# Performance work log

Hardware: AMD Instinct MI355X
Metric: run time of the kernel (lower is better)

Reference implementation:

```python
import jax, jax.numpy as jnp
import numpy as np

N, E, IN, H, OUT, G = 50000, 800000, 128, 256, 10, 512


def setup_inputs() -> dict:
    key = jax.random.key(0)
    ks = jax.random.split(key, 12)
    def lin(k, fan_in, fan_out):
        s = 1.0 / np.sqrt(fan_in)
        kw, kb = jax.random.split(k)
        W = jax.random.uniform(kw, (fan_in, fan_out), jnp.float32, -s, s)
        b = jax.random.uniform(kb, (fan_out,), jnp.float32, -s, s)
        return W, b
    x = jax.random.normal(ks[0], (N, IN), jnp.float32)
    edge_index = jax.random.randint(ks[1], (2, E), 0, N)
    batch = jnp.sort(jax.random.randint(ks[2], (N,), 0, G))
    W1a, b1a = lin(ks[3], IN, H)
    W1b, b1b = lin(ks[4], H, H)
    W2a, b2a = lin(ks[5], H, H)
    W2b, b2b = lin(ks[6], H, H)
    Wlin, blin = lin(ks[7], H, OUT)
    eps1 = jnp.zeros((), jnp.float32)
    eps2 = jnp.zeros((), jnp.float32)
    return dict(x=x, edge_index=edge_index, batch=batch,
                eps1=eps1, W1a=W1a, b1a=b1a, W1b=W1b, b1b=b1b,
                eps2=eps2, W2a=W2a, b2a=b2a, W2b=W2b, b2b=b2b,
                Wlin=Wlin, blin=blin)


def reference(x, edge_index, batch, eps1, W1a, b1a, W1b, b1b,
              eps2, W2a, b2a, W2b, b2b, Wlin, blin):
    src, dst = edge_index[0], edge_index[1]
    # GINConv 1: h = MLP((1+eps)*x + sum_{j in N(i)} x_j)
    agg = jax.ops.segment_sum(x[src], dst, num_segments=N)  # [N, IN]
    h = (1.0 + eps1) * x + agg
    h = jax.nn.relu(h @ W1a + b1a) @ W1b + b1b              # [N, H]
    h = jax.nn.relu(h)  # (dropout p=0.3 is identity in eval mode)
    # GINConv 2
    agg2 = jax.ops.segment_sum(h[src], dst, num_segments=N)  # [N, H]
    h2 = (1.0 + eps2) * h + agg2
    h2 = jax.nn.relu(h2 @ W2a + b2a) @ W2b + b2b             # [N, H]
    # global mean pool per graph
    psum = jax.ops.segment_sum(h2, batch, num_segments=G)    # [G, H]
    cnt = jax.ops.segment_sum(jnp.ones((N, 1), h2.dtype), batch, num_segments=G)
    pooled = psum / jnp.maximum(cnt, 1.0)
    out = pooled @ Wlin + blin                               # [G, OUT]
    return jax.nn.log_softmax(out, axis=-1)
```

## Files before the change

### kernel.cpp

```cpp
#include <hip/hip_runtime.h>
#include <math.h>
#include <stdint.h>

constexpr int N   = 50000;
constexpr int E   = 800000;
constexpr int IN  = 128;
constexpr int H   = 256;
constexpr int OUT = 10;
constexpr int G   = 512;
constexpr int BSTR = 64;

constexpr int NPART  = 391;
constexpr int SEGCAP = 48;
constexpr int EPB    = 4096;
constexpr int AB     = (E + EPB - 1) / EPB;

typedef __bf16 bf16x8 __attribute__((ext_vector_type(8)));
typedef float  f32x4  __attribute__((ext_vector_type(4)));
typedef float  f32x2  __attribute__((ext_vector_type(2)));

__device__ __forceinline__ float blo(unsigned v) { return __uint_as_float(v << 16); }
__device__ __forceinline__ float bhi(unsigned v) { return __uint_as_float(v & 0xffff0000u); }
__device__ __forceinline__ unsigned short f2b(float f) {
  unsigned u = __float_as_uint(f);
  u += 0x7fffu + ((u >> 16) & 1u);
  return (unsigned short)(u >> 16);
}
__device__ __forceinline__ unsigned packb(float lo, float hi) {
  return (unsigned)f2b(lo) | ((unsigned)f2b(hi) << 16);
}
__device__ __forceinline__ unsigned pk_fp8x4(float a, float b, float c, float d) {
  int r = 0;
  r = __builtin_amdgcn_cvt_pk_fp8_f32(a, b, r, false);
  r = __builtin_amdgcn_cvt_pk_fp8_f32(c, d, r, true);
  return (unsigned)r;
}
__device__ __forceinline__ unsigned char fp8_1(float v) {
  return (unsigned char)(__builtin_amdgcn_cvt_pk_fp8_f32(v, v, 0, false) & 0xff);
}
__device__ __forceinline__ f32x2 upk_fp8(unsigned short s) {
  return __builtin_amdgcn_cvt_pk_f32_fp8((int)s, false);
}


constexpr int XQ_BLOCKS  = (N * IN / 4) / 256;
constexpr int W1A_BLOCKS = (256 * IN) / 256;
constexpr int WH_BLOCKS  = (256 * H) / 256;

__global__ __launch_bounds__(256) void prep_kernel(
    const int* __restrict__ srcp, const int* __restrict__ dstp,
    unsigned* __restrict__ pbuf, int* __restrict__ pcnt,
    const float* __restrict__ x, unsigned* __restrict__ xq,
    const float* __restrict__ W1a, unsigned short* __restrict__ Wt1a,
    const float* __restrict__ W1b, unsigned short* __restrict__ Wt1b,
    const float* __restrict__ W2a, unsigned short* __restrict__ Wt2a,
    const float* __restrict__ W2b, unsigned short* __restrict__ Wt2b) {
  __shared__ int lcur[NPART];
  int b = blockIdx.x;
  int t = threadIdx.x;
  if (b < AB) {
    for (int j = t; j < NPART; j += 256) lcur[j] = 0;
    __syncthreads();
    const int e0 = b * EPB;
#pragma unroll
    for (int r = 0; r < EPB / 1024; ++r) {
      int base = e0 + (r * 256 + t) * 4;
      if (base < E) {
        int4 d4 = *(const int4*)(dstp + base);
        int4 s4 = *(const int4*)(srcp + base);
        int dd[4] = {d4.x, d4.y, d4.z, d4.w};
        int ss[4] = {s4.x, s4.y, s4.z, s4.w};
#pragma unroll
        for (int u = 0; u < 4; ++u) {
          int part = dd[u] >> 7, dl = dd[u] & 127;
          int pos = atomicAdd(&lcur[part], 1);
          if (pos < SEGCAP)
            pbuf[((size_t)part * AB + b) * SEGCAP + pos] =
                ((unsigned)dl << 16) | (unsigned)ss[u];
        }
      }
    }
    __syncthreads();
    for (int j = t; j < NPART; j += 256) pcnt[b * NPART + j] = min(lcur[j], SEGCAP);
    return;
  }
  b -= AB;
  if (b < XQ_BLOCKS) {
    int id = b * 256 + t;
    float4 v = ((const float4*)x)[id];
    xq[id] = pk_fp8x4(v.x, v.y, v.z, v.w);
    return;
  }
  b -= XQ_BLOCKS;
  if (b < W1A_BLOCKS) {
    int id = b * 256 + t;
    int n = id >> 7, k = id & 127;
    Wt1a[id] = f2b(W1a[k * 256 + n]);
    return;
  }
  b -= W1A_BLOCKS;
  const float* Ws;
  unsigned short* Wd;
  if (b < WH_BLOCKS)            { Ws = W1b; Wd = Wt1b; }
  else if (b < 2 * WH_BLOCKS)   { Ws = W2a; Wd = Wt2a; b -= WH_BLOCKS; }
  else                          { Ws = W2b; Wd = Wt2b; b -= 2 * WH_BLOCKS; }
  int id = b * 256 + t;
  int n = id >> 8, k = id & 255;
  Wd[id] = f2b(Ws[k * 256 + n]);
}


__global__ __launch_bounds__(256) void csr_kernel(const unsigned* __restrict__ pbuf,
                                                  const int* __restrict__ pcnt,
                                                  int* __restrict__ deg, int* __restrict__ csre) {
  __shared__ int sa[256], sb[256];
  __shared__ int ldeg[128];
  int p = blockIdx.x;
  int t = threadIdx.x;
  if (t < 128) ldeg[t] = 0;
  sa[t] = (t < AB) ? pcnt[t * NPART + p] : 0;
  __syncthreads();
  int* cur = sa; int* nxt = sb;
#pragma unroll
  for (int off = 1; off < 256; off <<= 1) {
    nxt[t] = cur[t] + ((t >= off) ? cur[t - off] : 0);
    __syncthreads();
    int* tmp = cur; cur = nxt; nxt = tmp;
  }
  int T = cur[255];
  const unsigned* seg = pbuf + (size_t)p * AB * SEGCAP;
  for (int f = t; f < T; f += 256) {
    int lo = 0, hi = AB - 1;
    while (lo < hi) { int m = (lo + hi) >> 1; if (cur[m] > f) hi = m; else lo = m + 1; }
    int bb = lo;
    int excl = bb ? cur[bb - 1] : 0;
    unsigned v = seg[(size_t)bb * SEGCAP + (f - excl)];
    int dl = (int)(v >> 16), s = (int)(v & 0xFFFFu);
    int pos = atomicAdd(&ldeg[dl], 1);
    if (pos < BSTR) csre[(((size_t)p << 7) + dl) * BSTR + pos] = s;
  }
  __syncthreads();
  if (t < 128) {
    int node = (p << 7) + t;
    if (node < N) deg[node] = min(ldeg[t], BSTR);
  }
}


template <int RS>
__global__ __launch_bounds__(64) void agg_pair_kernel(
    const unsigned char* __restrict__ inq,
    const int* __restrict__ deg, const int* __restrict__ csre,
    const float* __restrict__ epsp, unsigned short* __restrict__ out) {
  constexpr int NPAIR = N / 2;
  int bx = blockIdx.x;
  int half = (RS == 256) ? (bx / NPAIR) : 0;
  int pair = (RS == 256) ? (bx - half * NPAIR) : bx;
  int lane = threadIdx.x;
  int hsel = lane >> 5;
  int l = lane & 31;
  int i = pair * 2 + hsel;
  int dg = deg[i]; if (dg > BSTR) dg = BSTR;
  const int* bkt = csre + (size_t)i * BSTR;
  int dgmax = max(dg, __shfl_xor(dg, 32));
  const unsigned char* rowbase = inq + half * 128 + l * 4;
  float a0 = 0.f, a1 = 0.f, a2 = 0.f, a3 = 0.f;
  int hi_j = dg - 1; if (hi_j < 0) hi_j = 0;
  for (int j = 0; j < dgmax; j += 8) {
    unsigned idx[8], v[8];
#pragma unroll
    for (int u = 0; u < 8; ++u) {
      int jc = j + u; if (jc > hi_j) jc = hi_j;
      unsigned raw = (unsigned)bkt[jc];
      idx[u] = raw < (unsigned)N ? raw : 0u;
    }
#pragma unroll
    for (int u = 0; u < 8; ++u) v[u] = *(const unsigned*)(rowbase + (size_t)idx[u] * RS);
#pragma unroll
    for (int u = 0; u < 8; ++u) {
      float s = (j + u < dg) ? 1.f : 0.f;
      f32x2 lo = __builtin_amdgcn_cvt_pk_f32_fp8((int)v[u], false);
      f32x2 hh = __builtin_amdgcn_cvt_pk_f32_fp8((int)v[u], true);
      a0 += s * lo.x; a1 += s * lo.y; a2 += s * hh.x; a3 += s * hh.y;
    }
  }
  float sc = 1.0f + epsp[0];
  unsigned sv = *(const unsigned*)(rowbase + (size_t)i * RS);
  f32x2 slo = __builtin_amdgcn_cvt_pk_f32_fp8((int)sv, false);
  f32x2 shi = __builtin_amdgcn_cvt_pk_f32_fp8((int)sv, true);
  a0 += sc * slo.x; a1 += sc * slo.y; a2 += sc * shi.x; a3 += sc * shi.y;
  unsigned short* orow = out + (size_t)i * RS + half * 128 + l * 4;
  *(uint2*)orow = make_uint2(packb(a0, a1), packb(a2, a3));
}


template <int K1, bool RELU2, bool OUT8>
__global__ __launch_bounds__(256, 2) void mlp_kernel(
    const unsigned short* __restrict__ A,
    const unsigned short* __restrict__ Bta,
    const float* __restrict__ ba,
    const unsigned short* __restrict__ Btb,
    const float* __restrict__ bb,
    void* __restrict__ outv, int Nrows) {
  constexpr int M = 256, LDK = 40, LDI = 168;
  __shared__ __align__(16) unsigned short sh[10240 + 21504];
  unsigned short* Bs = sh;
  unsigned short* Is = sh + 10240;
  unsigned short* As = sh + 10240;
  const int tid  = threadIdx.x;
  const int r0   = blockIdx.x * 128;
  const int wave = tid >> 6, lane = tid & 63;
  const int quad = lane >> 4, l15 = lane & 15;
  const int wrow = (wave >> 1) * 64, wcol = (wave & 1) * 64;
  const int srow = tid >> 2;
  const int sk8  = (tid & 3) * 8;

  f32x4 acc1[2][4][4];
#pragma unroll
  for (int c = 0; c < 2; ++c)
#pragma unroll
    for (int i = 0; i < 4; ++i)
#pragma unroll
      for (int j = 0; j < 4; ++j) acc1[c][i][j] = (f32x4){0.f, 0.f, 0.f, 0.f};

  for (int k0 = 0; k0 < K1; k0 += 32) {
    {
      int grow = r0 + srow;
      uint4 v = make_uint4(0u, 0u, 0u, 0u);
      if (grow < Nrows) v = *(const uint4*)(A + (size_t)grow * K1 + k0 + sk8);
      *(uint4*)(As + srow * LDK + sk8) = v;
      grow = r0 + srow + 64;
      uint4 w = make_uint4(0u, 0u, 0u, 0u);
      if (grow < Nrows) w = *(const uint4*)(A + (size_t)grow * K1 + k0 + sk8);
      *(uint4*)(As + (srow + 64) * LDK + sk8) = w;
#pragma unroll
      for (int sgm = 0; sgm < 4; ++sgm) {
        int col = srow + sgm * 64;
        *(uint4*)(Bs + col * LDK + sk8) = *(const uint4*)(Bta + (size_t)col * K1 + k0 + sk8);
      }
    }
    __syncthreads();
    bf16x8 af[4];
#pragma unroll
    for (int mt = 0; mt < 4; ++mt)
      af[mt] = *(const bf16x8*)(As + (wrow + mt * 16 + l15) * LDK + quad * 8);
#pragma unroll
    for (int ch = 0; ch < 2; ++ch) {
      bf16x8 bfr[4];
#pragma unroll
      for (int nt = 0; nt < 4; ++nt)
        bfr[nt] = *(const bf16x8*)(Bs + (ch * 128 + wcol + nt * 16 + l15) * LDK + quad * 8);
#pragma unroll
      for (int mt = 0; mt < 4; ++mt)
#pragma unroll
        for (int nt = 0; nt < 4; ++nt)
          acc1[ch][mt][nt] =
              __builtin_amdgcn_mfma_f32_16x16x32_bf16(af[mt], bfr[nt], acc1[ch][mt][nt], 0, 0, 0);
    }
    __syncthreads();
  }

  float bva[2][4];
#pragma unroll
  for (int c = 0; c < 2; ++c)
#pragma unroll
    for (int nt = 0; nt < 4; ++nt) bva[c][nt] = ba[c * 128 + wcol + nt * 16 + l15];

  f32x4 acc2[2][4][4];
#pragma unroll
  for (int c = 0; c < 2; ++c)
#pragma unroll
    for (int i = 0; i < 4; ++i)
#pragma unroll
      for (int j = 0; j < 4; ++j) acc2[c][i][j] = (f32x4){0.f, 0.f, 0.f, 0.f};

  for (int ch = 0; ch < 2; ++ch) {
    __syncthreads();
#pragma unroll
    for (int mt = 0; mt < 4; ++mt)
#pragma unroll
      for (int nt = 0; nt < 4; ++nt) {
        int col = wcol + nt * 16 + l15;
        int rbase = wrow + mt * 16 + quad * 4;
#pragma unroll
        for (int i = 0; i < 4; ++i)
          Is[(rbase + i) * LDI + col] = f2b(fmaxf(acc1[ch][mt][nt][i] + bva[ch][nt], 0.f));
      }
    for (int kk = 0; kk < 4; ++kk) {
      __syncthreads();
      {
        int k0 = ch * 128 + kk * 32;
#pragma unroll
        for (int sgm = 0; sgm < 4; ++sgm) {
          int col = srow + sgm * 64;
          *(uint4*)(Bs + col * LDK + sk8) = *(const uint4*)(Btb + (size_t)col * 256 + k0 + sk8);
        }
      }
      __syncthreads();
      bf16x8 af[4];
#pragma unroll
      for (int mt = 0; mt < 4; ++mt)
        af[mt] = *(const bf16x8*)(Is + (wrow + mt * 16 + l15) * LDI + kk * 32 + quad * 8);
#pragma unroll
      for (int c2 = 0; c2 < 2; ++c2) {
        bf16x8 bfr[4];
#pragma unroll
        for (int nt = 0; nt < 4; ++nt)
          bfr[nt] = *(const bf16x8*)(Bs + (c2 * 128 + wcol + nt * 16 + l15) * LDK + quad * 8);
#pragma unroll
        for (int mt = 0; mt < 4; ++mt)
#pragma unroll
          for (int nt = 0; nt < 4; ++nt)
            acc2[c2][mt][nt] =
                __builtin_amdgcn_mfma_f32_16x16x32_bf16(af[mt], bfr[nt], acc2[c2][mt][nt], 0, 0, 0);
      }
    }
    __syncthreads();
  }

#pragma unroll
  for (int c2 = 0; c2 < 2; ++c2) {
    float bv[4];
#pragma unroll
    for (int nt = 0; nt < 4; ++nt) bv[nt] = bb[c2 * 128 + wcol + nt * 16 + l15];
#pragma unroll
    for (int mt = 0; mt < 4; ++mt) {
      int gr0 = r0 + wrow + mt * 16 + quad * 4;
#pragma unroll
      for (int i = 0; i < 4; ++i) {
        int grow = gr0 + i;
        if (grow >= Nrows) continue;
#pragma unroll
        for (int nt = 0; nt < 4; ++nt) {
          float v = acc2[c2][mt][nt][i] + bv[nt];
          if (RELU2) v = fmaxf(v, 0.f);
          int col = c2 * 128 + wcol + nt * 16 + l15;
          if (OUT8) ((unsigned char*)outv)[(size_t)grow * M + col] = fp8_1(v);
          else      ((unsigned short*)outv)[(size_t)grow * M + col] = f2b(v);
        }
      }
    }
  }
}


__global__ __launch_bounds__(128) void pool_final_kernel(const unsigned short* __restrict__ h2,
                                                         const int* __restrict__ batch,
                                                         const float* __restrict__ Wlin,
                                                         const float* __restrict__ blin,
                                                         float* __restrict__ out) {
  __shared__ float sp[H];
  __shared__ float logits[OUT];
  int g = blockIdx.x;
  int t = threadIdx.x;
  int lo = 0, hi = N;
  while (lo < hi) { int m = (lo + hi) >> 1; if (batch[m] < g) lo = m + 1; else hi = m; }
  int s = lo;
  lo = 0; hi = N;
  while (lo < hi) { int m = (lo + hi) >> 1; if (batch[m] < g + 1) lo = m + 1; else hi = m; }
  int e = lo;
  float a0 = 0.f, a1 = 0.f;
  const unsigned* base = (const unsigned*)h2;
  int n = s;
  for (; n + 4 <= e; n += 4) {
    unsigned v0 = base[(size_t)(n + 0) * (H / 2) + t];
    unsigned v1 = base[(size_t)(n + 1) * (H / 2) + t];
    unsigned v2 = base[(size_t)(n + 2) * (H / 2) + t];
    unsigned v3 = base[(size_t)(n + 3) * (H / 2) + t];
    a0 += blo(v0) + blo(v1) + blo(v2) + blo(v3);
    a1 += bhi(v0) + bhi(v1) + bhi(v2) + bhi(v3);
  }
  for (; n < e; ++n) {
    unsigned v = base[(size_t)n * (H / 2) + t];
    a0 += blo(v); a1 += bhi(v);
  }
  float inv = 1.0f / fmaxf((float)(e - s), 1.0f);
  sp[2 * t]     = a0 * inv;
  sp[2 * t + 1] = a1 * inv;
  __syncthreads();
  if (t < OUT) {
    float acc = blin[t];
    for (int k = 0; k < H; ++k) acc = fmaf(sp[k], Wlin[k * OUT + t], acc);
    logits[t] = acc;
  }
  __syncthreads();
  if (t == 0) {
    float m = -INFINITY;
    for (int j = 0; j < OUT; ++j) m = fmaxf(m, logits[j]);
    float ssum = 0.f;
    for (int j = 0; j < OUT; ++j) ssum += expf(logits[j] - m);
    float ls = logf(ssum);
    for (int j = 0; j < OUT; ++j) out[(size_t)g * OUT + j] = logits[j] - m - ls;
  }
}


static inline char* align_up(char* p, size_t a) {
  return (char*)(((uintptr_t)p + a - 1) & ~(a - 1));
}

extern "C" void kernel_launch(void* const* d_in, const int* in_sizes, int n_in,
                              void* d_out, int out_size, void* d_ws, size_t ws_size,
                              hipStream_t stream) {
  const float* x    = (const float*)d_in[0];
  const int*   ei   = (const int*)d_in[1];
  const int*   srcp = ei;
  const int*   dstp = ei + E;
  const int*   batch = (const int*)d_in[2];
  const float* eps1 = (const float*)d_in[3];
  const float* W1a  = (const float*)d_in[4];
  const float* b1a  = (const float*)d_in[5];
  const float* W1b  = (const float*)d_in[6];
  const float* b1b  = (const float*)d_in[7];
  const float* eps2 = (const float*)d_in[8];
  const float* W2a  = (const float*)d_in[9];
  const float* b2a  = (const float*)d_in[10];
  const float* W2b  = (const float*)d_in[11];
  const float* b2b  = (const float*)d_in[12];
  const float* Wlin = (const float*)d_in[13];
  const float* blin = (const float*)d_in[14];
  float* outp = (float*)d_out;

  char* p = (char*)d_ws;
  unsigned* pbuf = (unsigned*)p;     p = align_up(p + (size_t)NPART * AB * SEGCAP * 4, 256);
  int* pcnt = (int*)p;               p = align_up(p + (size_t)AB * NPART * 4, 256);
  int* deg  = (int*)p;               p = align_up(p + (size_t)N * 4, 256);
  int* csre = (int*)p;               p = align_up(p + (size_t)NPART * 128 * BSTR * 4, 256);
  unsigned* xq = (unsigned*)p;       p = align_up(p + (size_t)N * IN, 256);
  unsigned char* h1q = (unsigned char*)p;  p = align_up(p + (size_t)N * H, 256);
  unsigned short* B1 = (unsigned short*)p; p = align_up(p + (size_t)N * IN * 2, 256);
  unsigned short* B2 = (unsigned short*)p; p = align_up(p + (size_t)N * H * 2, 256);
  unsigned short* B3 = (unsigned short*)p; p = align_up(p + (size_t)N * H * 2, 256);
  unsigned short* Wt1a = (unsigned short*)p;  p = align_up(p + (size_t)H * IN * 2, 256);
  unsigned short* Wt1b = (unsigned short*)p;  p = align_up(p + (size_t)H * H * 2, 256);
  unsigned short* Wt2a = (unsigned short*)p;  p = align_up(p + (size_t)H * H * 2, 256);
  unsigned short* Wt2b = (unsigned short*)p;  p = align_up(p + (size_t)H * H * 2, 256);

  prep_kernel<<<AB + XQ_BLOCKS + W1A_BLOCKS + 3 * WH_BLOCKS, 256, 0, stream>>>(
      srcp, dstp, pbuf, pcnt, x, xq, W1a, Wt1a, W1b, Wt1b, W2a, Wt2a, W2b, Wt2b);

  csr_kernel<<<NPART, 256, 0, stream>>>(pbuf, pcnt, deg, csre);

  const int ggrid = (N + 127) / 128;

  agg_pair_kernel<IN><<<N / 2, 64, 0, stream>>>((const unsigned char*)xq, deg, csre, eps1, B1);
  mlp_kernel<IN, true, true><<<ggrid, 256, 0, stream>>>(B1, Wt1a, b1a, Wt1b, b1b, h1q, N);

  agg_pair_kernel<H><<<N, 64, 0, stream>>>(h1q, deg, csre, eps2, B3);
  mlp_kernel<H, false, false><<<ggrid, 256, 0, stream>>>(B3, Wt2a, b2a, Wt2b, b2b, B2, N);

  pool_final_kernel<<<G, 128, 0, stream>>>(B2, batch, Wlin, blin, outp);
}
```

Measured before the change: 253.3 us.

## Fuse neighbor aggregation into MLP kernel, gathering rows directly into shared memory

Removes the separate agg_pair kernels and their bf16 intermediate buffers. Each MLP block now gathers FP8 neighbor rows for its 64 nodes, sums them, writes the bf16 result straight into an LDS A-tile, and then runs the two GEMMs. The row tile shrinks from 128 to 64 nodes and each thread now gathers 32-byte chunks of a row. This saves global round trips and two launches, at the cost of a larger LDS footprint and of the gather latency sitting inside the GEMM block, where it may limit overlap and occupancy.

```diff
diff --git a/kernel.cpp b/kernel.cpp
--- a/kernel.cpp
+++ b/kernel.cpp
@@ -38,8 +38,18 @@
 __device__ __forceinline__ unsigned char fp8_1(float v) {
   return (unsigned char)(__builtin_amdgcn_cvt_pk_fp8_f32(v, v, 0, false) & 0xff);
 }
-__device__ __forceinline__ f32x2 upk_fp8(unsigned short s) {
-  return __builtin_amdgcn_cvt_pk_f32_fp8((int)s, false);
+
+__device__ __forceinline__ void acc16(float* a, uint4 w, float s) {
+  unsigned ws[4] = {w.x, w.y, w.z, w.w};
+#pragma unroll
+  for (int d = 0; d < 4; ++d) {
+    f32x2 lo = __builtin_amdgcn_cvt_pk_f32_fp8((int)ws[d], false);
+    f32x2 hi = __builtin_amdgcn_cvt_pk_f32_fp8((int)ws[d], true);
+    a[4*d+0] = fmaf(s, lo.x, a[4*d+0]);
+    a[4*d+1] = fmaf(s, lo.y, a[4*d+1]);
+    a[4*d+2] = fmaf(s, hi.x, a[4*d+2]);
+    a[4*d+3] = fmaf(s, hi.y, a[4*d+3]);
+  }
 }
 
 
@@ -147,103 +157,103 @@
 }
 
 
-template <int RS>
-__global__ __launch_bounds__(64) void agg_pair_kernel(
+template <int K1, bool RELU2, bool OUT8>
+__global__ __launch_bounds__(256, 2) void fused_mlp_kernel(
     const unsigned char* __restrict__ inq,
     const int* __restrict__ deg, const int* __restrict__ csre,
-    const float* __restrict__ epsp, unsigned short* __restrict__ out) {
-  constexpr int NPAIR = N / 2;
-  int bx = blockIdx.x;
-  int half = (RS == 256) ? (bx / NPAIR) : 0;
-  int pair = (RS == 256) ? (bx - half * NPAIR) : bx;
-  int lane = threadIdx.x;
-  int hsel = lane >> 5;
-  int l = lane & 31;
-  int i = pair * 2 + hsel;
-  int dg = deg[i]; if (dg > BSTR) dg = BSTR;
-  const int* bkt = csre + (size_t)i * BSTR;
-  int dgmax = max(dg, __shfl_xor(dg, 32));
-  const unsigned char* rowbase = inq + half * 128 + l * 4;
-  float a0 = 0.f, a1 = 0.f, a2 = 0.f, a3 = 0.f;
-  int hi_j = dg - 1; if (hi_j < 0) hi_j = 0;
-  for (int j = 0; j < dgmax; j += 8) {
-    unsigned idx[8], v[8];
-#pragma unroll
-    for (int u = 0; u < 8; ++u) {
-      int jc = j + u; if (jc > hi_j) jc = hi_j;
-      unsigned raw = (unsigned)bkt[jc];
-      idx[u] = raw < (unsigned)N ? raw : 0u;
-    }
-#pragma unroll
-    for (int u = 0; u < 8; ++u) v[u] = *(const unsigned*)(rowbase + (size_t)idx[u] * RS);
-#pragma unroll
-    for (int u = 0; u < 8; ++u) {
-      float s = (j + u < dg) ? 1.f : 0.f;
-      f32x2 lo = __builtin_amdgcn_cvt_pk_f32_fp8((int)v[u], false);
-      f32x2 hh = __builtin_amdgcn_cvt_pk_f32_fp8((int)v[u], true);
-      a0 += s * lo.x; a1 += s * lo.y; a2 += s * hh.x; a3 += s * hh.y;
-    }
-  }
-  float sc = 1.0f + epsp[0];
-  unsigned sv = *(const unsigned*)(rowbase + (size_t)i * RS);
-  f32x2 slo = __builtin_amdgcn_cvt_pk_f32_fp8((int)sv, false);
-  f32x2 shi = __builtin_amdgcn_cvt_pk_f32_fp8((int)sv, true);
-  a0 += sc * slo.x; a1 += sc * slo.y; a2 += sc * shi.x; a3 += sc * shi.y;
-  unsigned short* orow = out + (size_t)i * RS + half * 128 + l * 4;
-  *(uint2*)orow = make_uint2(packb(a0, a1), packb(a2, a3));
-}
-
-
-template <int K1, bool RELU2, bool OUT8>
-__global__ __launch_bounds__(256, 2) void mlp_kernel(
-    const unsigned short* __restrict__ A,
+    const float* __restrict__ epsp,
     const unsigned short* __restrict__ Bta,
     const float* __restrict__ ba,
     const unsigned short* __restrict__ Btb,
     const float* __restrict__ bb,
     void* __restrict__ outv, int Nrows) {
-  constexpr int M = 256, LDK = 40, LDI = 168;
-  __shared__ __align__(16) unsigned short sh[10240 + 21504];
+  constexpr int LDK = 40, LDI = 168;
+  constexpr int LDA = K1 + 40;
+  constexpr int TPN = K1 / 32;
+  constexpr int NPP = 256 / TPN;
+  constexpr int PASSES = 64 / NPP;
+  __shared__ __align__(16) unsigned short sh[10240 + 64 * LDA];
   unsigned short* Bs = sh;
+  unsigned short* Af = sh + 10240;
   unsigned short* Is = sh + 10240;
-  unsigned short* As = sh + 10240;
   const int tid  = threadIdx.x;
-  const int r0   = blockIdx.x * 128;
+  const int r0   = blockIdx.x * 64;
   const int wave = tid >> 6, lane = tid & 63;
   const int quad = lane >> 4, l15 = lane & 15;
-  const int wrow = (wave >> 1) * 64, wcol = (wave & 1) * 64;
+  const int wrow = (wave >> 1) * 32, wcol = (wave & 1) * 64;
   const int srow = tid >> 2;
   const int sk8  = (tid & 3) * 8;
 
-  f32x4 acc1[2][4][4];
+  {
+    const float sc = 1.0f + epsp[0];
+    const int slot = tid % TPN;
+    const int nd0  = tid / TPN;
+    const unsigned char* rb = inq + slot * 32;
+#pragma unroll
+    for (int ps = 0; ps < PASSES; ++ps) {
+      const int node = ps * NPP + nd0;
+      const int i = r0 + node;
+      float a[32];
+#pragma unroll
+      for (int q = 0; q < 32; ++q) a[q] = 0.f;
+      if (i < Nrows) {
+        int dg = deg[i]; if (dg > BSTR) dg = BSTR;
+        const int* bkt = csre + (size_t)i * BSTR;
+        int j = 0;
+        for (; j + 4 <= dg; j += 4) {
+          uint4 v[8];
+#pragma unroll
+          for (int u = 0; u < 4; ++u) {
+            unsigned raw = (unsigned)bkt[j + u];
+            if (raw >= (unsigned)N) raw = 0u;
+            const uint4* src = (const uint4*)(rb + (size_t)raw * K1);
+            v[2*u]   = src[0];
+            v[2*u+1] = src[1];
+          }
+#pragma unroll
+          for (int u = 0; u < 4; ++u) {
+            acc16(a,      v[2*u],   1.0f);
+            acc16(a + 16, v[2*u+1], 1.0f);
+          }
+        }
+        for (; j < dg; ++j) {
+          unsigned raw = (unsigned)bkt[j];
+          if (raw >= (unsigned)N) raw = 0u;
+          const uint4* src = (const uint4*)(rb + (size_t)raw * K1);
+          acc16(a, src[0], 1.0f);
+          acc16(a + 16, src[1], 1.0f);
+        }
+        const uint4* sr = (const uint4*)(rb + (size_t)i * K1);
+        acc16(a, sr[0], sc);
+        acc16(a + 16, sr[1], sc);
+      }
+      uint4* dst = (uint4*)(Af + node * LDA + slot * 32);
+#pragma unroll
+      for (int w = 0; w < 4; ++w)
+        dst[w] = make_uint4(packb(a[8*w+0], a[8*w+1]), packb(a[8*w+2], a[8*w+3]),
+                            packb(a[8*w+4], a[8*w+5]), packb(a[8*w+6], a[8*w+7]));
+    }
+  }
+
+  f32x4 acc1[2][2][4];
 #pragma unroll
   for (int c = 0; c < 2; ++c)
 #pragma unroll
-    for (int i = 0; i < 4; ++i)
+    for (int i = 0; i < 2; ++i)
 #pragma unroll
       for (int j = 0; j < 4; ++j) acc1[c][i][j] = (f32x4){0.f, 0.f, 0.f, 0.f};
 
   for (int k0 = 0; k0 < K1; k0 += 32) {
-    {
-      int grow = r0 + srow;
-      uint4 v = make_uint4(0u, 0u, 0u, 0u);
-      if (grow < Nrows) v = *(const uint4*)(A + (size_t)grow * K1 + k0 + sk8);
-      *(uint4*)(As + srow * LDK + sk8) = v;
-      grow = r0 + srow + 64;
-      uint4 w = make_uint4(0u, 0u, 0u, 0u);
-      if (grow < Nrows) w = *(const uint4*)(A + (size_t)grow * K1 + k0 + sk8);
-      *(uint4*)(As + (srow + 64) * LDK + sk8) = w;
-#pragma unroll
-      for (int sgm = 0; sgm < 4; ++sgm) {
-        int col = srow + sgm * 64;
-        *(uint4*)(Bs + col * LDK + sk8) = *(const uint4*)(Bta + (size_t)col * K1 + k0 + sk8);
-      }
-    }
-    __syncthreads();
-    bf16x8 af[4];
-#pragma unroll
-    for (int mt = 0; mt < 4; ++mt)
-      af[mt] = *(const bf16x8*)(As + (wrow + mt * 16 + l15) * LDK + quad * 8);
+#pragma unroll
+    for (int sgm = 0; sgm < 4; ++sgm) {
+      int col = srow + sgm * 64;
+      *(uint4*)(Bs + col * LDK + sk8) = *(const uint4*)(Bta + (size_t)col * K1 + k0 + sk8);
+    }
+    __syncthreads();
+    bf16x8 af[2];
+#pragma unroll
+    for (int mt = 0; mt < 2; ++mt)
+      af[mt] = *(const bf16x8*)(Af + (wrow + mt * 16 + l15) * LDA + k0 + quad * 8);
 #pragma unroll
     for (int ch = 0; ch < 2; ++ch) {
       bf16x8 bfr[4];
@@ -251,7 +261,7 @@
       for (int nt = 0; nt < 4; ++nt)
         bfr[nt] = *(const bf16x8*)(Bs + (ch * 128 + wcol + nt * 16 + l15) * LDK + quad * 8);
 #pragma unroll
-      for (int mt = 0; mt < 4; ++mt)
+      for (int mt = 0; mt < 2; ++mt)
 #pragma unroll
         for (int nt = 0; nt < 4; ++nt)
           acc1[ch][mt][nt] =
@@ -266,18 +276,18 @@
 #pragma unroll
     for (int nt = 0; nt < 4; ++nt) bva[c][nt] = ba[c * 128 + wcol + nt * 16 + l15];
 
-  f32x4 acc2[2][4][4];
+  f32x4 acc2[2][2][4];
 #pragma unroll
   for (int c = 0; c < 2; ++c)
 #pragma unroll
-    for (int i = 0; i < 4; ++i)
+    for (int i = 0; i < 2; ++i)
 #pragma unroll
       for (int j = 0; j < 4; ++j) acc2[c][i][j] = (f32x4){0.f, 0.f, 0.f, 0.f};
 
   for (int ch = 0; ch < 2; ++ch) {
     __syncthreads();
 #pragma unroll
-    for (int mt = 0; mt < 4; ++mt)
+    for (int mt = 0; mt < 2; ++mt)
 #pragma unroll
       for (int nt = 0; nt < 4; ++nt) {
         int col = wcol + nt * 16 + l15;
@@ -297,9 +307,9 @@
         }
       }
       __syncthreads();
-      bf16x8 af[4];
-#pragma unroll
-      for (int mt = 0; mt < 4; ++mt)
+      bf16x8 af[2];
+#pragma unroll
+      for (int mt = 0; mt < 2; ++mt)
         af[mt] = *(const bf16x8*)(Is + (wrow + mt * 16 + l15) * LDI + kk * 32 + quad * 8);
 #pragma unroll
       for (int c2 = 0; c2 < 2; ++c2) {
@@ -308,7 +318,7 @@
         for (int nt = 0; nt < 4; ++nt)
           bfr[nt] = *(const bf16x8*)(Bs + (c2 * 128 + wcol + nt * 16 + l15) * LDK + quad * 8);
 #pragma unroll
-        for (int mt = 0; mt < 4; ++mt)
+        for (int mt = 0; mt < 2; ++mt)
 #pragma unroll
           for (int nt = 0; nt < 4; ++nt)
             acc2[c2][mt][nt] =
@@ -324,7 +334,7 @@
 #pragma unroll
     for (int nt = 0; nt < 4; ++nt) bv[nt] = bb[c2 * 128 + wcol + nt * 16 + l15];
 #pragma unroll
-    for (int mt = 0; mt < 4; ++mt) {
+    for (int mt = 0; mt < 2; ++mt) {
       int gr0 = r0 + wrow + mt * 16 + quad * 4;
 #pragma unroll
       for (int i = 0; i < 4; ++i) {
@@ -335,8 +345,8 @@
           float v = acc2[c2][mt][nt][i] + bv[nt];
           if (RELU2) v = fmaxf(v, 0.f);
           int col = c2 * 128 + wcol + nt * 16 + l15;
-          if (OUT8) ((unsigned char*)outv)[(size_t)grow * M + col] = fp8_1(v);
-          else      ((unsigned short*)outv)[(size_t)grow * M + col] = f2b(v);
+          if (OUT8) ((unsigned char*)outv)[(size_t)grow * 256 + col] = fp8_1(v);
+          else      ((unsigned short*)outv)[(size_t)grow * 256 + col] = f2b(v);
         }
       }
     }
@@ -428,9 +438,7 @@
   int* csre = (int*)p;               p = align_up(p + (size_t)NPART * 128 * BSTR * 4, 256);
   unsigned* xq = (unsigned*)p;       p = align_up(p + (size_t)N * IN, 256);
   unsigned char* h1q = (unsigned char*)p;  p = align_up(p + (size_t)N * H, 256);
-  unsigned short* B1 = (unsigned short*)p; p = align_up(p + (size_t)N * IN * 2, 256);
   unsigned short* B2 = (unsigned short*)p; p = align_up(p + (size_t)N * H * 2, 256);
-  unsigned short* B3 = (unsigned short*)p; p = align_up(p + (size_t)N * H * 2, 256);
   unsigned short* Wt1a = (unsigned short*)p;  p = align_up(p + (size_t)H * IN * 2, 256);
   unsigned short* Wt1b = (unsigned short*)p;  p = align_up(p + (size_t)H * H * 2, 256);
   unsigned short* Wt2a = (unsigned short*)p;  p = align_up(p + (size_t)H * H * 2, 256);
@@ -441,13 +449,13 @@
 
   csr_kernel<<<NPART, 256, 0, stream>>>(pbuf, pcnt, deg, csre);
 
-  const int ggrid = (N + 127) / 128;
-
-  agg_pair_kernel<IN><<<N / 2, 64, 0, stream>>>((const unsigned char*)xq, deg, csre, eps1, B1);
-  mlp_kernel<IN, true, true><<<ggrid, 256, 0, stream>>>(B1, Wt1a, b1a, Wt1b, b1b, h1q, N);
-
-  agg_pair_kernel<H><<<N, 64, 0, stream>>>(h1q, deg, csre, eps2, B3);
-  mlp_kernel<H, false, false><<<ggrid, 256, 0, stream>>>(B3, Wt2a, b2a, Wt2b, b2b, B2, N);
+  const int nb = (N + 63) / 64;
+
+  fused_mlp_kernel<IN, true, true><<<nb, 256, 0, stream>>>(
+      (const unsigned char*)xq, deg, csre, eps1, Wt1a, b1a, Wt1b, b1b, h1q, N);
+
+  fused_mlp_kernel<H, false, false><<<nb, 256, 0, stream>>>(
+      h1q, deg, csre, eps2, Wt2a, b2a, Wt2b, b2b, B2, N);
 
   pool_final_kernel<<<G, 128, 0, stream>>>(B2, batch, Wlin, blin, outp);
 }
```

New measurement: 258.3 us. No clear change (+2.0%).
